# Optimization experiments

Measured on AMD Instinct MI355X. Metric: run time of the kernel, lower is better.

Reference implementation:

```python
import jax, jax.numpy as jnp
import numpy as np

LAMBDA_FREQ = 0.1
LOWPASS_RATIO = 0.25
EPS_RATIO = 0.05
H_SPATIAL = 128
W_SPATIAL = 128


def _crps_pointwise(pred, target):
    # pred: (B, M, C, G); target: (B, C, G)
    M = pred.shape[1]
    eps = EPS_RATIO / M
    mae = jnp.abs(pred - target[:, None]).mean(axis=1)  # (B, C, G)
    term1 = mae.mean()
    # pairwise |p_i - p_j|: (B, M, M, C, G); diagonal is exactly 0 already
    pairwise = jnp.abs(pred[:, :, None] - pred[:, None, :])
    spread = pairwise.sum(axis=2) / (M - 1)  # (B, M, C, G)
    term2 = spread.mean() * (1.0 - eps)
    return term1 - 0.5 * term2


def _lowpass_fft(x):
    # x: (B, M, C, H, W) -> complex (B, M, C, H, W//2+1), low-pass masked
    X = jnp.fft.rfft2(x, axes=(-2, -1))
    Hf, Wf = X.shape[-2], X.shape[-1]
    cut_h = max(int(Hf * LOWPASS_RATIO), 1)
    cut_w = max(int(Wf * LOWPASS_RATIO), 1)
    mask = jnp.zeros((Hf, Wf), dtype=bool).at[:cut_h, :cut_w].set(True)
    return X * mask


def setup_inputs() -> dict:
    key = jax.random.key(0)
    k1, k2 = jax.random.split(key)
    target = jax.random.normal(k1, (8, 3, H_SPATIAL, W_SPATIAL), dtype=jnp.float32)
    output = jax.random.normal(k2, (8, 16, 3, H_SPATIAL, W_SPATIAL), dtype=jnp.float32)
    return {"target": target, "output": output}


def reference(target, output):
    B, M, C = output.shape[0], output.shape[1], output.shape[2]
    target_flat = target.reshape(B, C, -1)           # (B, C, G)
    output_flat = output.reshape(B, M, C, -1)        # (B, M, C, G)
    crps_p = _crps_pointwise(output_flat, target_flat)

    out_fft = _lowpass_fft(output).reshape(B, M, C, -1)             # (B, M, C, Gf)
    tgt_fft = _lowpass_fft(target[:, None]).reshape(B, C, -1)       # (B, C, Gf)
    crps_f = _crps_pointwise(jnp.abs(out_fft), jnp.abs(tgt_fft))

    return crps_p + LAMBDA_FREQ * crps_f
```

## Files before the change

kernel.cpp:

```cpp
#include <hip/hip_runtime.h>
#include <math.h>

#define NB 8
#define NM 16
#define NC 3
#define NH 128
#define NW 128
#define NG (NH * NW)
#define NGF (NH * (NW / 2 + 1))
#define NKH 32
#define NKW 16
#define NK (NKH * NKW)
#define N_PRED_IMG (NB * NM * NC)
#define N_IMG (N_PRED_IMG + NB * NC)

#define PT_BLOCKS 384
#define FQ_BLOCKS 48

#define WS_PP_OFF 0
#define WS_FP_OFF (PT_BLOCKS * 16)
#define WS_MAG_OFF 7168
#define WS_MAG_BYTES (N_IMG * NK * 4)
#define WS_Y_OFF (WS_MAG_OFF + WS_MAG_BYTES)

__global__ __launch_bounds__(256) void crps_point_kernel(
    const float* __restrict__ pred,
    const float* __restrict__ tgt,
    double2* __restrict__ pp) {
  int tid = threadIdx.x;
  int i4 = (blockIdx.x * 256 + tid) * 4;
  int b = i4 / (NC * NG);
  int cg = i4 - b * (NC * NG);
  const float* base = pred + (size_t)b * (NM * NC * NG) + cg;
  float4 t = *(const float4*)&tgt[i4];
  float4 p[NM];
#pragma unroll
  for (int m = 0; m < NM; ++m)
    p[m] = *(const float4*)&base[(size_t)m * (NC * NG)];

  float s1 = 0.f, s2 = 0.f;
#pragma unroll
  for (int m = 0; m < NM; ++m) {
    s1 += fabsf(p[m].x - t.x) + fabsf(p[m].y - t.y) +
          fabsf(p[m].z - t.z) + fabsf(p[m].w - t.w);
  }
#pragma unroll
  for (int m = 0; m < NM; ++m)
#pragma unroll
    for (int j = m + 1; j < NM; ++j) {
      s2 += fabsf(p[m].x - p[j].x) + fabsf(p[m].y - p[j].y) +
            fabsf(p[m].z - p[j].z) + fabsf(p[m].w - p[j].w);
    }

  for (int off = 32; off > 0; off >>= 1) {
    s1 += __shfl_down(s1, off);
    s2 += __shfl_down(s2, off);
  }
  __shared__ float ls1[4], ls2[4];
  if ((tid & 63) == 0) { ls1[tid >> 6] = s1; ls2[tid >> 6] = s2; }
  __syncthreads();
  if (tid == 0) {
    double a = 0.0, c = 0.0;
#pragma unroll
    for (int w = 0; w < 4; ++w) { a += (double)ls1[w]; c += (double)ls2[w]; }
    pp[blockIdx.x] = make_double2(a, c);
  }
}

__global__ __launch_bounds__(256) void dft_rows_kernel(
    const float* __restrict__ pred,
    const float* __restrict__ tgt,
    float2* __restrict__ Y) {
  __shared__ float2 roots[NW];
  int t = threadIdx.x;
  if (t < NW) {
    float ang = -2.0f * 3.14159265358979323846f * (float)t / (float)NW;
    float s, c;
    sincosf(ang, &s, &c);
    roots[t] = make_float2(c, s);
  }
  __syncthreads();

  int i = blockIdx.x * 256 + t;
  int img = i >> 11;
  int rem = i & 2047;
  int h = rem >> 4;
  int kw = rem & 15;
  const float* src =
      ((img < N_PRED_IMG) ? pred + (size_t)img * NG
                          : tgt + (size_t)(img - N_PRED_IMG) * NG) +
      h * NW;
  float ax = 0.f, ay = 0.f;
  int idx = 0;
#pragma unroll 8
  for (int w = 0; w < NW; ++w) {
    float v = src[w];
    float2 r = roots[idx];
    ax = fmaf(v, r.x, ax);
    ay = fmaf(v, r.y, ay);
    idx = (idx + kw) & (NW - 1);
  }
  Y[i] = make_float2(ax, ay);
}

__global__ __launch_bounds__(256) void dft_cols_mag_kernel(
    const float2* __restrict__ Y,
    float* __restrict__ mag) {
  __shared__ float2 roots[NH];
  int t = threadIdx.x;
  if (t < NH) {
    float ang = -2.0f * 3.14159265358979323846f * (float)t / (float)NH;
    float s, c;
    sincosf(ang, &s, &c);
    roots[t] = make_float2(c, s);
  }
  __syncthreads();

  int i = blockIdx.x * 256 + t;
  int img = i >> 9;
  int rem = i & 511;
  int kh = rem >> 4;
  int kw = rem & 15;
  const float2* ybase = Y + (size_t)img * (NH * NKW) + kw;
  float ax = 0.f, ay = 0.f;
  int idx = 0;
#pragma unroll 4
  for (int h = 0; h < NH; ++h) {
    float2 y = ybase[h * NKW];
    float2 r = roots[idx];
    ax += y.x * r.x - y.y * r.y;
    ay += y.x * r.y + y.y * r.x;
    idx = (idx + kh) & (NH - 1);
  }
  mag[i] = sqrtf(ax * ax + ay * ay);
}

__global__ __launch_bounds__(256) void crps_freq_kernel(
    const float* __restrict__ mag,
    double2* __restrict__ fp) {
  int tid = threadIdx.x;
  int i = blockIdx.x * 256 + tid;
  int b = i / (NC * NK);
  int rem = i - b * (NC * NK);
  const float* pb = mag + (size_t)b * (NM * NC * NK) + rem;
  float t = mag[(size_t)N_PRED_IMG * NK + (size_t)b * (NC * NK) + rem];
  float p[NM];
#pragma unroll
  for (int m = 0; m < NM; ++m) p[m] = pb[(size_t)m * (NC * NK)];
  float s1 = 0.f, s2 = 0.f;
#pragma unroll
  for (int m = 0; m < NM; ++m) s1 += fabsf(p[m] - t);
#pragma unroll
  for (int m = 0; m < NM; ++m)
#pragma unroll
    for (int j = m + 1; j < NM; ++j) s2 += fabsf(p[m] - p[j]);
  for (int off = 32; off > 0; off >>= 1) {
    s1 += __shfl_down(s1, off);
    s2 += __shfl_down(s2, off);
  }
  __shared__ float ls1[4], ls2[4];
  if ((tid & 63) == 0) { ls1[tid >> 6] = s1; ls2[tid >> 6] = s2; }
  __syncthreads();
  if (tid == 0) {
    double a = 0.0, c = 0.0;
#pragma unroll
    for (int w = 0; w < 4; ++w) { a += (double)ls1[w]; c += (double)ls2[w]; }
    fp[blockIdx.x] = make_double2(a, c);
  }
}

__global__ __launch_bounds__(256) void finalize_kernel(
    const double2* __restrict__ pp,
    const double2* __restrict__ fp,
    float* __restrict__ out) {
  int tid = threadIdx.x;
  double s1p = 0.0, s2p = 0.0, s1f = 0.0, s2f = 0.0;
  for (int j = tid; j < PT_BLOCKS; j += 256) {
    double2 v = pp[j]; s1p += v.x; s2p += v.y;
  }
  if (tid < FQ_BLOCKS) { double2 v = fp[tid]; s1f += v.x; s2f += v.y; }
  for (int off = 32; off > 0; off >>= 1) {
    s1p += __shfl_down(s1p, off);
    s2p += __shfl_down(s2p, off);
    s1f += __shfl_down(s1f, off);
    s2f += __shfl_down(s2f, off);
  }
  __shared__ double l[4][4];
  if ((tid & 63) == 0) {
    int w = tid >> 6;
    l[w][0] = s1p; l[w][1] = s2p; l[w][2] = s1f; l[w][3] = s2f;
  }
  __syncthreads();
  if (tid == 0) {
    double a0 = 0, a1 = 0, a2 = 0, a3 = 0;
#pragma unroll
    for (int w = 0; w < 4; ++w) {
      a0 += l[w][0]; a1 += l[w][1]; a2 += l[w][2]; a3 += l[w][3];
    }
    const double Bd = NB, Md = NM, Cd = NC, Gd = NG, Gfd = NGF;
    const double eps = 0.05 / Md;
    double term1_p = a0 / (Bd * Cd * Gd * Md);
    double term2_p = (1.0 - eps) * 2.0 * a1 / ((Md - 1.0) * Bd * Md * Cd * Gd);
    double crps_p = term1_p - 0.5 * term2_p;
    double term1_f = a2 / (Bd * Cd * Gfd * Md);
    double term2_f = (1.0 - eps) * 2.0 * a3 / ((Md - 1.0) * Bd * Md * Cd * Gfd);
    double crps_f = term1_f - 0.5 * term2_f;
    out[0] = (float)(crps_p + 0.1 * crps_f);
  }
}

extern "C" void kernel_launch(void* const* d_in, const int* in_sizes, int n_in,
                              void* d_out, int out_size, void* d_ws, size_t ws_size,
                              hipStream_t stream) {
  (void)in_sizes; (void)n_in; (void)out_size; (void)ws_size;
  const float* tgt = (const float*)d_in[0];
  const float* pred = (const float*)d_in[1];
  float* out = (float*)d_out;

  char* ws = (char*)d_ws;
  double2* pp = (double2*)(ws + WS_PP_OFF);
  double2* fp = (double2*)(ws + WS_FP_OFF);
  float* mag = (float*)(ws + WS_MAG_OFF);
  float2* Y = (float2*)(ws + WS_Y_OFF);

  crps_point_kernel<<<PT_BLOCKS, 256, 0, stream>>>(pred, tgt, pp);
  dft_rows_kernel<<<(N_IMG * NH * NKW) / 256, 256, 0, stream>>>(pred, tgt, Y);
  dft_cols_mag_kernel<<<(N_IMG * NK) / 256, 256, 0, stream>>>(Y, mag);
  crps_freq_kernel<<<FQ_BLOCKS, 256, 0, stream>>>(mag, fp);
  finalize_kernel<<<1, 256, 0, stream>>>(pp, fp, out);
}
```

Before: 110.5 us.

## Fuse point CRPS and per-image 2D DFT into one kernel, fold finalize

```diff
diff --git a/kernel.cpp b/kernel.cpp
--- a/kernel.cpp
+++ b/kernel.cpp
@@ -17,128 +17,140 @@
 #define PT_BLOCKS 384
 #define FQ_BLOCKS 48
 
-#define WS_PP_OFF 0
-#define WS_FP_OFF (PT_BLOCKS * 16)
+#define WS_PP_OFF  0
+#define WS_FP_OFF  6144
+#define WS_CTR_OFF 6912
 #define WS_MAG_OFF 7168
-#define WS_MAG_BYTES (N_IMG * NK * 4)
-#define WS_Y_OFF (WS_MAG_OFF + WS_MAG_BYTES)
-
-__global__ __launch_bounds__(256) void crps_point_kernel(
+
+#define PI_F 3.14159265358979323846f
+
+__global__ __launch_bounds__(256) void fused_main_kernel(
     const float* __restrict__ pred,
     const float* __restrict__ tgt,
-    double2* __restrict__ pp) {
-  int tid = threadIdx.x;
-  int i4 = (blockIdx.x * 256 + tid) * 4;
-  int b = i4 / (NC * NG);
-  int cg = i4 - b * (NC * NG);
-  const float* base = pred + (size_t)b * (NM * NC * NG) + cg;
-  float4 t = *(const float4*)&tgt[i4];
-  float4 p[NM];
-#pragma unroll
-  for (int m = 0; m < NM; ++m)
-    p[m] = *(const float4*)&base[(size_t)m * (NC * NG)];
-
-  float s1 = 0.f, s2 = 0.f;
-#pragma unroll
-  for (int m = 0; m < NM; ++m) {
-    s1 += fabsf(p[m].x - t.x) + fabsf(p[m].y - t.y) +
-          fabsf(p[m].z - t.z) + fabsf(p[m].w - t.w);
-  }
-#pragma unroll
-  for (int m = 0; m < NM; ++m)
-#pragma unroll
-    for (int j = m + 1; j < NM; ++j) {
-      s2 += fabsf(p[m].x - p[j].x) + fabsf(p[m].y - p[j].y) +
-            fabsf(p[m].z - p[j].z) + fabsf(p[m].w - p[j].w);
-    }
-
-  for (int off = 32; off > 0; off >>= 1) {
-    s1 += __shfl_down(s1, off);
-    s2 += __shfl_down(s2, off);
-  }
+    double2* __restrict__ pp,
+    float* __restrict__ mag,
+    unsigned* __restrict__ ctr) {
+  __shared__ float4 xs4[32 * 33];
+  __shared__ float2 Yl[NH * NKW];
+  __shared__ float2 roots[NH];
   __shared__ float ls1[4], ls2[4];
-  if ((tid & 63) == 0) { ls1[tid >> 6] = s1; ls2[tid >> 6] = s2; }
-  __syncthreads();
-  if (tid == 0) {
-    double a = 0.0, c = 0.0;
-#pragma unroll
-    for (int w = 0; w < 4; ++w) { a += (double)ls1[w]; c += (double)ls2[w]; }
-    pp[blockIdx.x] = make_double2(a, c);
-  }
-}
-
-__global__ __launch_bounds__(256) void dft_rows_kernel(
-    const float* __restrict__ pred,
-    const float* __restrict__ tgt,
-    float2* __restrict__ Y) {
-  __shared__ float2 roots[NW];
-  int t = threadIdx.x;
-  if (t < NW) {
-    float ang = -2.0f * 3.14159265358979323846f * (float)t / (float)NW;
-    float s, c;
-    sincosf(ang, &s, &c);
-    roots[t] = make_float2(c, s);
-  }
-  __syncthreads();
-
-  int i = blockIdx.x * 256 + t;
-  int img = i >> 11;
-  int rem = i & 2047;
-  int h = rem >> 4;
-  int kw = rem & 15;
-  const float* src =
-      ((img < N_PRED_IMG) ? pred + (size_t)img * NG
-                          : tgt + (size_t)(img - N_PRED_IMG) * NG) +
-      h * NW;
-  float ax = 0.f, ay = 0.f;
-  int idx = 0;
-#pragma unroll 8
-  for (int w = 0; w < NW; ++w) {
-    float v = src[w];
-    float2 r = roots[idx];
-    ax = fmaf(v, r.x, ax);
-    ay = fmaf(v, r.y, ay);
-    idx = (idx + kw) & (NW - 1);
-  }
-  Y[i] = make_float2(ax, ay);
-}
-
-__global__ __launch_bounds__(256) void dft_cols_mag_kernel(
-    const float2* __restrict__ Y,
-    float* __restrict__ mag) {
-  __shared__ float2 roots[NH];
-  int t = threadIdx.x;
+
+  const int t = threadIdx.x;
+  const int blk = blockIdx.x;
+
+  if (blk < PT_BLOCKS) {
+    if (blk == 0 && t == 0) *ctr = 0;
+    int i4 = (blk * 256 + t) * 4;
+    int b = i4 / (NC * NG);
+    int cg = i4 - b * (NC * NG);
+    const float* base = pred + (size_t)b * (NM * NC * NG) + cg;
+    float4 tv = *(const float4*)&tgt[i4];
+    float4 p[NM];
+#pragma unroll
+    for (int m = 0; m < NM; ++m)
+      p[m] = *(const float4*)&base[(size_t)m * (NC * NG)];
+
+    float s1 = 0.f, s2 = 0.f;
+#pragma unroll
+    for (int m = 0; m < NM; ++m)
+      s1 += fabsf(p[m].x - tv.x) + fabsf(p[m].y - tv.y) +
+            fabsf(p[m].z - tv.z) + fabsf(p[m].w - tv.w);
+#pragma unroll
+    for (int m = 0; m < NM; ++m)
+#pragma unroll
+      for (int j = m + 1; j < NM; ++j)
+        s2 += fabsf(p[m].x - p[j].x) + fabsf(p[m].y - p[j].y) +
+              fabsf(p[m].z - p[j].z) + fabsf(p[m].w - p[j].w);
+
+    for (int off = 32; off > 0; off >>= 1) {
+      s1 += __shfl_down(s1, off);
+      s2 += __shfl_down(s2, off);
+    }
+    if ((t & 63) == 0) { ls1[t >> 6] = s1; ls2[t >> 6] = s2; }
+    __syncthreads();
+    if (t == 0) {
+      double a = 0.0, c = 0.0;
+#pragma unroll
+      for (int w = 0; w < 4; ++w) { a += (double)ls1[w]; c += (double)ls2[w]; }
+      pp[blk] = make_double2(a, c);
+    }
+    return;
+  }
+
+  const int img = blk - PT_BLOCKS;
+  const float* src = (img < N_PRED_IMG)
+                         ? pred + (size_t)img * NG
+                         : tgt + (size_t)(img - N_PRED_IMG) * NG;
+  const float4* src4 = (const float4*)src;
+
   if (t < NH) {
-    float ang = -2.0f * 3.14159265358979323846f * (float)t / (float)NH;
-    float s, c;
-    sincosf(ang, &s, &c);
-    roots[t] = make_float2(c, s);
-  }
-  __syncthreads();
-
-  int i = blockIdx.x * 256 + t;
-  int img = i >> 9;
-  int rem = i & 511;
-  int kh = rem >> 4;
-  int kw = rem & 15;
-  const float2* ybase = Y + (size_t)img * (NH * NKW) + kw;
-  float ax = 0.f, ay = 0.f;
+    float ang = -2.0f * PI_F * (float)t / (float)NH;
+    float sv, cv;
+    sincosf(ang, &sv, &cv);
+    roots[t] = make_float2(cv, sv);
+  }
+  __syncthreads();
+
+  const int kw = t & 15, r2 = t >> 4;
+  for (int c = 0; c < 4; ++c) {
+#pragma unroll
+    for (int j = 0; j < 4; ++j) {
+      int p = j * 256 + t;
+      float4 v = src4[c * 1024 + p];
+      xs4[(p >> 5) * 33 + (p & 31)] = v;
+    }
+    __syncthreads();
+
+    float ax1 = 0.f, ay1 = 0.f, ax2 = 0.f, ay2 = 0.f;
+    int idx = 0;
+    const float4* rowA = &xs4[r2 * 33];
+    const float4* rowB = &xs4[(r2 + 16) * 33];
+#pragma unroll 4
+    for (int w4 = 0; w4 < 32; ++w4) {
+      float4 a = rowA[w4];
+      float4 bb = rowB[w4];
+      float2 rt;
+      rt = roots[idx]; idx = (idx + kw) & 127;
+      ax1 = fmaf(a.x, rt.x, ax1); ay1 = fmaf(a.x, rt.y, ay1);
+      ax2 = fmaf(bb.x, rt.x, ax2); ay2 = fmaf(bb.x, rt.y, ay2);
+      rt = roots[idx]; idx = (idx + kw) & 127;
+      ax1 = fmaf(a.y, rt.x, ax1); ay1 = fmaf(a.y, rt.y, ay1);
+      ax2 = fmaf(bb.y, rt.x, ax2); ay2 = fmaf(bb.y, rt.y, ay2);
+      rt = roots[idx]; idx = (idx + kw) & 127;
+      ax1 = fmaf(a.z, rt.x, ax1); ay1 = fmaf(a.z, rt.y, ay1);
+      ax2 = fmaf(bb.z, rt.x, ax2); ay2 = fmaf(bb.z, rt.y, ay2);
+      rt = roots[idx]; idx = (idx + kw) & 127;
+      ax1 = fmaf(a.w, rt.x, ax1); ay1 = fmaf(a.w, rt.y, ay1);
+      ax2 = fmaf(bb.w, rt.x, ax2); ay2 = fmaf(bb.w, rt.y, ay2);
+    }
+    Yl[(c * 32 + r2) * NKW + kw] = make_float2(ax1, ay1);
+    Yl[(c * 32 + r2 + 16) * NKW + kw] = make_float2(ax2, ay2);
+    __syncthreads();
+  }
+
+  const int kh = t >> 3, kwb = t & 7;
+  float axA = 0.f, ayA = 0.f, axB = 0.f, ayB = 0.f;
   int idx = 0;
 #pragma unroll 4
   for (int h = 0; h < NH; ++h) {
-    float2 y = ybase[h * NKW];
-    float2 r = roots[idx];
-    ax += y.x * r.x - y.y * r.y;
-    ay += y.x * r.y + y.y * r.x;
-    idx = (idx + kh) & (NH - 1);
-  }
-  mag[i] = sqrtf(ax * ax + ay * ay);
+    float2 rt = roots[idx]; idx = (idx + kh) & 127;
+    float2 ya = Yl[h * NKW + kwb];
+    float2 yb = Yl[h * NKW + kwb + 8];
+    axA += ya.x * rt.x - ya.y * rt.y; ayA += ya.x * rt.y + ya.y * rt.x;
+    axB += yb.x * rt.x - yb.y * rt.y; ayB += yb.x * rt.y + yb.y * rt.x;
+  }
+  float* mo = mag + (size_t)img * NK;
+  mo[kh * NKW + kwb] = sqrtf(axA * axA + ayA * ayA);
+  mo[kh * NKW + kwb + 8] = sqrtf(axB * axB + ayB * ayB);
 }
 
-__global__ __launch_bounds__(256) void crps_freq_kernel(
+__global__ __launch_bounds__(256) void crps_freq_final_kernel(
     const float* __restrict__ mag,
-    double2* __restrict__ fp) {
-  int tid = threadIdx.x;
+    const double2* __restrict__ pp,
+    double2* __restrict__ fp,
+    unsigned* __restrict__ ctr,
+    float* __restrict__ out) {
+  const int tid = threadIdx.x;
   int i = blockIdx.x * 256 + tid;
   int b = i / (NC * NK);
   int rem = i - b * (NC * NK);
@@ -159,6 +171,7 @@
     s2 += __shfl_down(s2, off);
   }
   __shared__ float ls1[4], ls2[4];
+  __shared__ int sLast;
   if ((tid & 63) == 0) { ls1[tid >> 6] = s1; ls2[tid >> 6] = s2; }
   __syncthreads();
   if (tid == 0) {
@@ -166,14 +179,14 @@
 #pragma unroll
     for (int w = 0; w < 4; ++w) { a += (double)ls1[w]; c += (double)ls2[w]; }
     fp[blockIdx.x] = make_double2(a, c);
-  }
-}
-
-__global__ __launch_bounds__(256) void finalize_kernel(
-    const double2* __restrict__ pp,
-    const double2* __restrict__ fp,
-    float* __restrict__ out) {
-  int tid = threadIdx.x;
+    __threadfence();
+    unsigned old = atomicAdd(ctr, 1u);
+    sLast = (old == FQ_BLOCKS - 1);
+  }
+  __syncthreads();
+  if (!sLast) return;
+  __threadfence();
+
   double s1p = 0.0, s2p = 0.0, s1f = 0.0, s2f = 0.0;
   for (int j = tid; j < PT_BLOCKS; j += 256) {
     double2 v = pp[j]; s1p += v.x; s2p += v.y;
@@ -220,12 +233,9 @@
   char* ws = (char*)d_ws;
   double2* pp = (double2*)(ws + WS_PP_OFF);
   double2* fp = (double2*)(ws + WS_FP_OFF);
+  unsigned* ctr = (unsigned*)(ws + WS_CTR_OFF);
   float* mag = (float*)(ws + WS_MAG_OFF);
-  float2* Y = (float2*)(ws + WS_Y_OFF);
-
-  crps_point_kernel<<<PT_BLOCKS, 256, 0, stream>>>(pred, tgt, pp);
-  dft_rows_kernel<<<(N_IMG * NH * NKW) / 256, 256, 0, stream>>>(pred, tgt, Y);
-  dft_cols_mag_kernel<<<(N_IMG * NK) / 256, 256, 0, stream>>>(Y, mag);
-  crps_freq_kernel<<<FQ_BLOCKS, 256, 0, stream>>>(mag, fp);
-  finalize_kernel<<<1, 256, 0, stream>>>(pp, fp, out);
+
+  fused_main_kernel<<<PT_BLOCKS + N_IMG, 256, 0, stream>>>(pred, tgt, pp, mag, ctr);
+  crps_freq_final_kernel<<<FQ_BLOCKS, 256, 0, stream>>>(mag, pp, fp, ctr, out);
 }
```

New measurement: 102.4 us. 7.2% less time.
